# Optimization experiments

Measured on AMD Instinct MI355X. Metric: run time of the kernel, lower is better.

Reference implementation:

```python
import jax, jax.numpy as jnp
import numpy as np

D_MODEL, D_HEAD, N_HEADS, N_KV_HEADS = 4096, 128, 32, 8
EPS = 1e-5
N = 2048


def rms_norm(x, w, eps):
    return x * jax.lax.rsqrt(jnp.mean(x * x, axis=-1, keepdims=True) + eps) * w


def rope_swap(x):
    # [x0, x1, x2, x3] -> [-x1, x0, -x3, x2]
    xp = x.reshape(x.shape[:-1] + (-1, 2))
    return jnp.stack([-xp[..., 1], xp[..., 0]], axis=-1).reshape(x.shape)


def rope_rotate(x, r_cos, r_sin):
    return x * r_cos + rope_swap(x) * r_sin


def setup_inputs() -> dict:
    key = jax.random.key(0)
    ks = jax.random.split(key, 8)
    sd = 1.0 / np.sqrt(D_MODEL)
    return {
        "x": jax.random.normal(ks[0], (N, D_MODEL), dtype=jnp.float32),
        "r_cos": jax.random.normal(ks[1], (N, D_HEAD), dtype=jnp.float32),
        "r_sin": jax.random.normal(ks[2], (N, D_HEAD), dtype=jnp.float32),
        "w_norm": jnp.ones((D_MODEL,), dtype=jnp.float32),
        "wq": jax.random.normal(ks[3], (D_MODEL, N_HEADS * D_HEAD), dtype=jnp.float32) * sd,
        "wk": jax.random.normal(ks[4], (D_MODEL, N_KV_HEADS * D_HEAD), dtype=jnp.float32) * sd,
        "wv": jax.random.normal(ks[5], (D_MODEL, N_KV_HEADS * D_HEAD), dtype=jnp.float32) * sd,
        "wo": jax.random.normal(ks[6], (D_MODEL, D_MODEL), dtype=jnp.float32) * sd,
    }


def reference(x, r_cos, r_sin, w_norm, wq, wk, wv, wo):
    n = x.shape[0]
    residual = x
    h = rms_norm(x, w_norm, EPS)

    # projections -> [n_heads, n, d_head]
    q = (h @ wq).reshape(n, N_HEADS, D_HEAD).transpose(1, 0, 2)
    k = (h @ wk).reshape(n, N_KV_HEADS, D_HEAD).transpose(1, 0, 2)
    v = (h @ wv).reshape(n, N_KV_HEADS, D_HEAD).transpose(1, 0, 2)

    # GQA: repeat kv heads
    reps = N_HEADS // N_KV_HEADS
    k = jnp.repeat(k, reps, axis=0)
    v = jnp.repeat(v, reps, axis=0)

    q = rope_rotate(q, r_cos, r_sin)
    k = rope_rotate(k, r_cos, r_sin)

    mask = jnp.where(
        jnp.tril(jnp.ones((n, n), dtype=bool)), 0.0, -jnp.inf
    ).astype(x.dtype)
    scores = jnp.einsum("hnd,hmd->hnm", q, k) / np.sqrt(D_HEAD).astype(np.float32) + mask
    a = jnp.einsum("hnm,hmd->hnd", jax.nn.softmax(scores, axis=-1), v)

    a = a.transpose(1, 0, 2).reshape(n, N_HEADS * D_HEAD)
    return residual + a @ wo
```

## Files before the change

kernel.cpp:

```cpp
#include <hip/hip_runtime.h>
#include <stdint.h>
#include <math.h>

#define TOK 2048
#define DMODEL 4096
#define QKV_LD 5120
#define KVB 64
#define PS_LD 72

typedef __attribute__((ext_vector_type(8))) short short8;
typedef __attribute__((ext_vector_type(4))) short short4v;
typedef __attribute__((ext_vector_type(8))) __bf16 bf16x8;
typedef __attribute__((ext_vector_type(4))) float f32x4;

__device__ __forceinline__ unsigned short f2bf(float f) {
  unsigned u = __float_as_uint(f);
  u += 0x7fffu + ((u >> 16) & 1u);
  return (unsigned short)(u >> 16);
}

__device__ __forceinline__ void gl16(const void* g, void* l) {
  __builtin_amdgcn_global_load_lds((__attribute__((address_space(1))) void*)g,
                                   (__attribute__((address_space(3))) void*)l,
                                   16, 0, 0);
}

__device__ __forceinline__ f32x4 mfma16(short8 a, short8 b, f32x4 c) {
  return __builtin_amdgcn_mfma_f32_16x16x32_bf16(__builtin_bit_cast(bf16x8, a),
                                                 __builtin_bit_cast(bf16x8, b),
                                                 c, 0, 0, 0);
}

__device__ __forceinline__ float fexp2(float x) {
  float r;
  asm("v_exp_f32 %0, %1" : "=v"(r) : "v"(x));
  return r;
}

template <int N>
__device__ __forceinline__ void waitvm() {
  if constexpr (N == 0) asm volatile("s_waitcnt vmcnt(0)" ::: "memory");
  else if constexpr (N == 3) asm volatile("s_waitcnt vmcnt(3)" ::: "memory");
  else if constexpr (N == 4) asm volatile("s_waitcnt vmcnt(4)" ::: "memory");
  else if constexpr (N == 8) asm volatile("s_waitcnt vmcnt(8)" ::: "memory");
  else static_assert(N == 0 || N == 3 || N == 4 || N == 8, "add literal");
}

__global__ __launch_bounds__(256) void k_rmsnorm(const float* __restrict__ x,
                                                 const float* __restrict__ w,
                                                 unsigned short* __restrict__ h) {
  const int row = blockIdx.x;
  const float* xr = x + (size_t)row * DMODEL;
  float4 v[4];
  float ss = 0.f;
#pragma unroll
  for (int i = 0; i < 4; ++i) {
    v[i] = *(const float4*)(xr + threadIdx.x * 4 + i * 1024);
    ss += v[i].x * v[i].x + v[i].y * v[i].y + v[i].z * v[i].z + v[i].w * v[i].w;
  }
#pragma unroll
  for (int m = 1; m < 64; m <<= 1) ss += __shfl_xor(ss, m, 64);
  __shared__ float ws4[4];
  if ((threadIdx.x & 63) == 0) ws4[threadIdx.x >> 6] = ss;
  __syncthreads();
  const float scale = rsqrtf((ws4[0] + ws4[1] + ws4[2] + ws4[3]) * (1.0f / DMODEL) + 1e-5f);
  unsigned short* hr = h + (size_t)row * DMODEL;
#pragma unroll
  for (int i = 0; i < 4; ++i) {
    int col = threadIdx.x * 4 + i * 1024;
    float4 wv = *(const float4*)(w + col);
    uint2 o;
    o.x = (unsigned)f2bf(v[i].x * scale * wv.x) | ((unsigned)f2bf(v[i].y * scale * wv.y) << 16);
    o.y = (unsigned)f2bf(v[i].z * scale * wv.z) | ((unsigned)f2bf(v[i].w * scale * wv.w) << 16);
    *(uint2*)(hr + col) = o;
  }
}

__global__ __launch_bounds__(256) void k_wconvert(const float* __restrict__ W,
                                                  unsigned short* __restrict__ WT,
                                                  int K, int N) {
  __shared__ unsigned short tile[64][65];
  const int n0 = blockIdx.x * 64, k0 = blockIdx.y * 64;
  const int t = threadIdx.x;
  {
    const int r = t >> 2, c0 = (t & 3) * 16;
    const float* src = W + (size_t)(k0 + r) * N + n0 + c0;
#pragma unroll
    for (int i = 0; i < 4; ++i) {
      float4 f = *(const float4*)(src + i * 4);
      tile[r][c0 + i * 4 + 0] = f2bf(f.x);
      tile[r][c0 + i * 4 + 1] = f2bf(f.y);
      tile[r][c0 + i * 4 + 2] = f2bf(f.z);
      tile[r][c0 + i * 4 + 3] = f2bf(f.w);
    }
  }
  __syncthreads();
  {
    const int n = t >> 2, c0 = (t & 3) * 16;
    unsigned short* dst = WT + (size_t)(n0 + n) * K + k0 + c0;
    unsigned short v[16];
#pragma unroll
    for (int i = 0; i < 16; ++i) v[i] = tile[c0 + i][n];
    uint4 o0, o1;
    o0.x = v[0] | ((unsigned)v[1] << 16);  o0.y = v[2] | ((unsigned)v[3] << 16);
    o0.z = v[4] | ((unsigned)v[5] << 16);  o0.w = v[6] | ((unsigned)v[7] << 16);
    o1.x = v[8] | ((unsigned)v[9] << 16);  o1.y = v[10] | ((unsigned)v[11] << 16);
    o1.z = v[12] | ((unsigned)v[13] << 16); o1.w = v[14] | ((unsigned)v[15] << 16);
    *(uint4*)dst = o0;
    *(uint4*)(dst + 8) = o1;
  }
}

__device__ __forceinline__ short8 rdfrag(const unsigned short* buf, int row, int kc) {
  return *(const short8*)((const char*)buf + row * 128 + ((kc ^ (row & 7)) << 4));
}

template <int BM, int BN, int HALF>
__device__ __forceinline__ void stage_half(const unsigned short* __restrict__ A,
                                           const unsigned short* __restrict__ BT,
                                           unsigned short* __restrict__ buf,
                                           int m0, int n0, int K, int kt, int tid) {
  constexpr int LA = BM / 64, LB = BN / 64;
  constexpr int H0A = LA / 2, H0B = (LB + 1) / 2;
  constexpr int A0 = HALF ? H0A : 0, A1 = HALF ? LA : H0A;
  constexpr int B0 = HALF ? H0B : 0, B1 = HALF ? LB : H0B;
  unsigned short* bbuf = buf + BM * 64;
#pragma unroll
  for (int i = A0; i < A1; ++i) {
    const int s = i * 512 + tid, row = s >> 3, ch = s & 7;
    gl16(A + (size_t)(m0 + row) * K + kt + ((ch ^ (row & 7)) << 3), (char*)buf + s * 16);
  }
#pragma unroll
  for (int i = B0; i < B1; ++i) {
    const int s = i * 512 + tid, row = s >> 3, ch = s & 7;
    gl16(BT + (size_t)(n0 + row) * K + kt + ((ch ^ (row & 7)) << 3), (char*)bbuf + s * 16);
  }
}

template <int BM, int BN, int MODE>
__global__ __launch_bounds__(512, 2) void k_gemm_big(const unsigned short* __restrict__ A,
                                                     const unsigned short* __restrict__ BT,
                                                     const float* __restrict__ resid,
                                                     void* __restrict__ Cout,
                                                     unsigned short* __restrict__ vtg,
                                                     const float* __restrict__ rc,
                                                     const float* __restrict__ rs,
                                                     int M, int N, int K) {
  extern __shared__ __align__(16) unsigned short lds[];
  constexpr int MREP = BM / 32;
  constexpr int NREP = BN / 64;
  constexpr int TILE = (BM + BN) * 64;
  constexpr int LA = BM / 64, LB = BN / 64;
  constexpr int H0 = LA / 2 + (LB + 1) / 2;

  const int tid = threadIdx.x, lane = tid & 63;
  const int w = tid >> 6, wm = w >> 2, wn = w & 3;
  const int lr = lane & 15, lh = lane >> 4;

  const int wg0 = blockIdx.x;
  const int xcd = wg0 & 7, l = wg0 >> 3;
  const int m0 = (((xcd >> 2) << 2) + (l >> 3)) * BM;
  const int n0 = (((xcd & 3) << 3) + (l & 7)) * BN;

  const f32x4 zf = {0.f, 0.f, 0.f, 0.f};
  f32x4 acc[MREP][NREP];
#pragma unroll
  for (int i = 0; i < MREP; ++i) {
#pragma unroll
    for (int j = 0; j < NREP; ++j) acc[i][j] = zf;
  }

  const int arow0 = wm * (BM / 2);
  const int brow0 = wn * (BN / 4);
  const int NT = K >> 6;
  int cur = 0;

  stage_half<BM, BN, 0>(A, BT, lds, m0, n0, K, 0, tid);
  stage_half<BM, BN, 1>(A, BT, lds, m0, n0, K, 0, tid);

  for (int t = 0; t < NT; ++t) {
    const unsigned short* abuf = lds + cur * TILE;
    const unsigned short* bbuf = abuf + BM * 64;
    unsigned short* nbuf = lds + (cur ^ 1) * TILE;
    const bool pre = (t + 1 < NT);
    const int ktn = (t + 1) << 6;

    short8 bfr[NREP], afr[4];
    if (pre) {
      stage_half<BM, BN, 0>(A, BT, nbuf, m0, n0, K, ktn, tid);
      waitvm<H0>();
    } else {
      waitvm<0>();
    }
    __builtin_amdgcn_s_barrier();
#pragma unroll
    for (int nr = 0; nr < NREP; ++nr) bfr[nr] = rdfrag(bbuf, brow0 + nr * 16 + lr, lh);
#pragma unroll
    for (int mi = 0; mi < 4; ++mi) afr[mi] = rdfrag(abuf, arow0 + mi * 16 + lr, lh);
    __builtin_amdgcn_s_setprio(1);
#pragma unroll
    for (int mi = 0; mi < 4; ++mi) {
#pragma unroll
      for (int nr = 0; nr < NREP; ++nr)
        acc[mi][nr] = mfma16(afr[mi], bfr[nr], acc[mi][nr]);
    }
    __builtin_amdgcn_s_setprio(0);
    if (pre) stage_half<BM, BN, 1>(A, BT, nbuf, m0, n0, K, ktn, tid);
#pragma unroll
    for (int mi = 0; mi < 4; ++mi) afr[mi] = rdfrag(abuf, arow0 + (4 + mi) * 16 + lr, lh);
    __builtin_amdgcn_s_setprio(1);
#pragma unroll
    for (int mi = 0; mi < 4; ++mi) {
#pragma unroll
      for (int nr = 0; nr < NREP; ++nr)
        acc[4 + mi][nr] = mfma16(afr[mi], bfr[nr], acc[4 + mi][nr]);
    }
    __builtin_amdgcn_s_setprio(0);
#pragma unroll
    for (int nr = 0; nr < NREP; ++nr) bfr[nr] = rdfrag(bbuf, brow0 + nr * 16 + lr, 4 + lh);
#pragma unroll
    for (int mi = 0; mi < 4; ++mi) afr[mi] = rdfrag(abuf, arow0 + mi * 16 + lr, 4 + lh);
    __builtin_amdgcn_s_setprio(1);
#pragma unroll
    for (int mi = 0; mi < 4; ++mi) {
#pragma unroll
      for (int nr = 0; nr < NREP; ++nr)
        acc[mi][nr] = mfma16(afr[mi], bfr[nr], acc[mi][nr]);
    }
    __builtin_amdgcn_s_setprio(0);
#pragma unroll
    for (int mi = 0; mi < 4; ++mi) afr[mi] = rdfrag(abuf, arow0 + (4 + mi) * 16 + lr, 4 + lh);
    asm volatile("s_waitcnt lgkmcnt(0)" ::: "memory");
    __builtin_amdgcn_s_barrier();
    __builtin_amdgcn_s_setprio(1);
#pragma unroll
    for (int mi = 0; mi < 4; ++mi) {
#pragma unroll
      for (int nr = 0; nr < NREP; ++nr)
        acc[4 + mi][nr] = mfma16(afr[mi], bfr[nr], acc[4 + mi][nr]);
    }
    __builtin_amdgcn_s_setprio(0);
    cur ^= 1;
  }

#pragma unroll
  for (int ai = 0; ai < MREP; ++ai) {
#pragma unroll
    for (int ni = 0; ni < NREP; ++ni) {
      const int colg = n0 + wn * (BN / 4) + ni * 16 + lr;
      const int rowg0 = m0 + wm * (BM / 2) + ai * 16 + 4 * lh;
      if (MODE == 1) {
#pragma unroll
        for (int r = 0; r < 4; ++r)
          ((float*)Cout)[(size_t)(rowg0 + r) * N + colg] =
              acc[ai][ni][r] + resid[(size_t)(rowg0 + r) * N + colg];
      } else if (colg >= 5120) {
        short4v o;
#pragma unroll
        for (int r = 0; r < 4; ++r) o[r] = (short)f2bf(acc[ai][ni][r]);
        *(short4v*)(vtg + (size_t)(colg - 5120) * TOK + rowg0) = o;
      } else {
        const int d = colg & 127;
#pragma unroll
        for (int r = 0; r < 4; ++r) {
          const int row = rowg0 + r;
          const float v = acc[ai][ni][r];
          const float p = __shfl_xor(v, 1, 64);
          const float c = rc[row * 128 + d];
          const float s = rs[row * 128 + d];
          const float y = (lr & 1) ? fmaf(p, s, v * c) : fmaf(-p, s, v * c);
          ((unsigned short*)Cout)[(size_t)row * QKV_LD + colg] = f2bf(y);
        }
      }
    }
  }
}

__global__ __launch_bounds__(256) void k_attn(const unsigned short* __restrict__ qkv,
                                              const unsigned short* __restrict__ vtg,
                                              unsigned short* __restrict__ aout) {
  extern __shared__ __align__(16) unsigned short sm[];
  unsigned short* const KsB = sm;
  unsigned short* const VtB = sm + 2 * KVB * 128;
  unsigned short* const Ps = sm + 4 * KVB * 128;
  const int head = blockIdx.y;
  const int hkv = head >> 2;
  const int tid = threadIdx.x, lane = tid & 63, w = tid >> 6;
  const int lr = lane & 15, lh = lane >> 4;
  const float scale2 = 0.08838834764831845f * 1.44269504088896340736f;
  const f32x4 zf = {0.f, 0.f, 0.f, 0.f};

  for (int half = 0; half < 2; ++half) {
    const int qt = half ? (31 - blockIdx.x) : blockIdx.x;
    const int q0 = qt * 64;

    short8 qf[4];
    {
      const unsigned short* qbase = qkv + (size_t)(q0 + w * 16 + lr) * QKV_LD + head * 128;
#pragma unroll
      for (int kd = 0; kd < 4; ++kd) qf[kd] = *(const short8*)(qbase + kd * 32 + lh * 8);
    }
    f32x4 oacc[8];
#pragma unroll
    for (int vt = 0; vt < 8; ++vt) oacc[vt] = zf;
    float Mr[4], Lr[4];
#pragma unroll
    for (int r = 0; r < 4; ++r) { Mr[r] = -INFINITY; Lr[r] = 0.f; }

    const int nt = qt + 1;
    int cur = 0;

    {
#pragma unroll
      for (int c = 0; c < 4; ++c) {
        const int s = c * 256 + w * 64 + lane;
        const int row = s >> 4, cp = s & 15;
        gl16(qkv + (size_t)row * QKV_LD + 4096 + hkv * 128 + ((cp ^ (row & 7)) * 8),
             (char*)KsB + (c * 256 + w * 64) * 16);
      }
#pragma unroll
      for (int c = 0; c < 4; ++c) {
        const int s = c * 256 + w * 64 + lane;
        const int row = s >> 3, cp = s & 7;
        gl16(vtg + (size_t)(hkv * 128 + row) * TOK + ((cp ^ (row & 7)) * 8),
             (char*)VtB + (c * 256 + w * 64) * 16);
      }
    }

    for (int t = 0; t < nt; ++t) {
      const unsigned short* Ks = KsB + cur * (KVB * 128);
      const unsigned short* Vt = VtB + cur * (128 * KVB);
      const int kv0 = t * KVB;
      if (t + 1 < nt) {
        unsigned short* Ksn = KsB + (cur ^ 1) * (KVB * 128);
        unsigned short* Vtn = VtB + (cur ^ 1) * (128 * KVB);
        const int kvn = (t + 1) * KVB;
#pragma unroll
        for (int c = 0; c < 4; ++c) {
          const int s = c * 256 + w * 64 + lane;
          const int row = s >> 4, cp = s & 15;
          gl16(qkv + (size_t)(kvn + row) * QKV_LD + 4096 + hkv * 128 + ((cp ^ (row & 7)) * 8),
               (char*)Ksn + (c * 256 + w * 64) * 16);
        }
#pragma unroll
        for (int c = 0; c < 4; ++c) {
          const int s = c * 256 + w * 64 + lane;
          const int row = s >> 3, cp = s & 7;
          gl16(vtg + (size_t)(hkv * 128 + row) * TOK + kvn + ((cp ^ (row & 7)) * 8),
               (char*)Vtn + (c * 256 + w * 64) * 16);
        }
        waitvm<8>();
      } else {
        waitvm<0>();
      }
      __builtin_amdgcn_s_barrier();

      f32x4 sacc[4];
#pragma unroll
      for (int ct = 0; ct < 4; ++ct) {
        sacc[ct] = zf;
        const int row = ct * 16 + lr;
#pragma unroll
        for (int kd = 0; kd < 4; ++kd) {
          const short8 kf = *(const short8*)((const char*)Ks + row * 256 +
                                             (((kd * 4 + lh) ^ (row & 7)) * 16));
          sacc[ct] = mfma16(qf[kd], kf, sacc[ct]);
        }
      }

      float scv[4], pv[4][4];
#pragma unroll
      for (int r = 0; r < 4; ++r) {
        const int qrow = q0 + w * 16 + 4 * lh + r;
        float s0 = sacc[0][r] * scale2;
        float s1 = sacc[1][r] * scale2;
        float s2 = sacc[2][r] * scale2;
        float s3 = sacc[3][r] * scale2;
        if (kv0 + lr > qrow) s0 = -INFINITY;
        if (kv0 + 16 + lr > qrow) s1 = -INFINITY;
        if (kv0 + 32 + lr > qrow) s2 = -INFINITY;
        if (kv0 + 48 + lr > qrow) s3 = -INFINITY;
        float tmax = fmaxf(fmaxf(s0, s1), fmaxf(s2, s3));
        tmax = fmaxf(tmax, __shfl_xor(tmax, 1, 16));
        tmax = fmaxf(tmax, __shfl_xor(tmax, 2, 16));
        tmax = fmaxf(tmax, __shfl_xor(tmax, 4, 16));
        tmax = fmaxf(tmax, __shfl_xor(tmax, 8, 16));
        const float mnew = fmaxf(Mr[r], tmax);
        const float sc = fexp2(Mr[r] - mnew);
        Mr[r] = mnew;
        const float p0 = fexp2(s0 - mnew);
        const float p1 = fexp2(s1 - mnew);
        const float p2 = fexp2(s2 - mnew);
        const float p3 = fexp2(s3 - mnew);
        float ps = (p0 + p1) + (p2 + p3);
        ps += __shfl_xor(ps, 1, 16);
        ps += __shfl_xor(ps, 2, 16);
        ps += __shfl_xor(ps, 4, 16);
        ps += __shfl_xor(ps, 8, 16);
        Lr[r] = Lr[r] * sc + ps;
        scv[r] = sc;
        pv[r][0] = p0; pv[r][1] = p1; pv[r][2] = p2; pv[r][3] = p3;
      }
#pragma unroll
      for (int vt = 0; vt < 8; ++vt) {
#pragma unroll
        for (int r = 0; r < 4; ++r) oacc[vt][r] *= scv[r];
      }

      unsigned short* pw = Ps + w * (16 * PS_LD);
#pragma unroll
      for (int r = 0; r < 4; ++r) {
#pragma unroll
        for (int ct = 0; ct < 4; ++ct)
          pw[(4 * lh + r) * PS_LD + ct * 16 + lr] = f2bf(pv[r][ct]);
      }
      asm volatile("s_waitcnt lgkmcnt(0)" ::: "memory");
      short8 pf[2];
      pf[0] = *(const short8*)(pw + lr * PS_LD + lh * 8);
      pf[1] = *(const short8*)(pw + lr * PS_LD + 32 + lh * 8);
      __builtin_amdgcn_s_setprio(1);
#pragma unroll
      for (int vt = 0; vt < 8; ++vt) {
        const int d = vt * 16 + lr;
#pragma unroll
        for (int kb = 0; kb < 2; ++kb) {
          const short8 vf = *(const short8*)((const char*)Vt + d * 128 +
                                             (((kb * 4 + lh) ^ (lr & 7)) * 16));
          oacc[vt] = mfma16(pf[kb], vf, oacc[vt]);
        }
      }
      __builtin_amdgcn_s_setprio(0);
      asm volatile("s_waitcnt lgkmcnt(0)" ::: "memory");
      __builtin_amdgcn_s_barrier();
      cur ^= 1;
    }

#pragma unroll
    for (int r = 0; r < 4; ++r) {
      const float inv = 1.0f / Lr[r];
      const size_t rowoff = (size_t)(q0 + w * 16 + 4 * lh + r) * DMODEL + head * 128;
#pragma unroll
      for (int vt = 0; vt < 8; ++vt)
        aout[rowoff + vt * 16 + lr] = f2bf(oacc[vt][r] * inv);
    }
  }
}

extern "C" void kernel_launch(void* const* d_in, const int* in_sizes, int n_in,
                              void* d_out, int out_size, void* d_ws, size_t ws_size,
                              hipStream_t stream) {
  (void)in_sizes; (void)n_in; (void)out_size; (void)ws_size;
  const float* x     = (const float*)d_in[0];
  const float* r_cos = (const float*)d_in[1];
  const float* r_sin = (const float*)d_in[2];
  const float* wnorm = (const float*)d_in[3];
  const float* wq    = (const float*)d_in[4];
  const float* wk    = (const float*)d_in[5];
  const float* wv    = (const float*)d_in[6];
  const float* wo    = (const float*)d_in[7];

  unsigned short* bufA = (unsigned short*)d_ws;
  unsigned short* qkvb = bufA + (size_t)TOK * DMODEL;
  unsigned short* wT   = qkvb + (size_t)TOK * QKV_LD;
  unsigned short* vtg  = wT + (size_t)6144 * DMODEL;

  hipFuncSetAttribute((const void*)k_gemm_big<256, 192, 0>,
                      hipFuncAttributeMaxDynamicSharedMemorySize, 4 * (256 + 192) * 64);
  hipFuncSetAttribute((const void*)k_gemm_big<256, 128, 1>,
                      hipFuncAttributeMaxDynamicSharedMemorySize, 4 * (256 + 128) * 64);
  const int attn_lds = 4 * KVB * 128 * 2 + 4 * 16 * PS_LD * 2;
  hipFuncSetAttribute((const void*)k_attn,
                      hipFuncAttributeMaxDynamicSharedMemorySize, attn_lds);

  k_rmsnorm<<<TOK, 256, 0, stream>>>(x, wnorm, bufA);
  k_wconvert<<<dim3(64, 64), 256, 0, stream>>>(wq, wT, DMODEL, 4096);
  k_wconvert<<<dim3(16, 64), 256, 0, stream>>>(wk, wT + (size_t)4096 * DMODEL, DMODEL, 1024);
  k_wconvert<<<dim3(16, 64), 256, 0, stream>>>(wv, wT + (size_t)5120 * DMODEL, DMODEL, 1024);
  k_gemm_big<256, 192, 0><<<dim3(256), 512, 4 * (256 + 192) * 64, stream>>>(
      bufA, wT, nullptr, qkvb, vtg, r_cos, r_sin, TOK, 6144, DMODEL);
  k_wconvert<<<dim3(64, 64), 256, 0, stream>>>(wo, wT, DMODEL, 4096);
  k_attn<<<dim3(16, 32), 256, attn_lds, stream>>>(qkvb, vtg, bufA);
  k_gemm_big<256, 128, 1><<<dim3(256), 512, 4 * (256 + 128) * 64, stream>>>(
      bufA, wT, x, d_out, nullptr, nullptr, nullptr, TOK, DMODEL, DMODEL);
}
```

Before: 325.8 us.

## Defer softmax rescaling with threshold, skip masking off-diagonal, defer row-sum reduction

Reworks the online softmax in the attention inner loop. The causal mask is now applied only on the diagonal tile. The running max is updated, and the output accumulator rescaled, only when some row's new max exceeds the stored max by more than 8 (log2 domain), checked wave-uniformly with __all. The per-row sum is kept as per-lane partials and reduced across lanes once at the end rather than every tile. This removes the shuffle reductions and the 32 multiplies per tile, at the cost of letting exp2 values grow up to 2^8 before rescaling, which bounds precision in bf16 P.

After: 309.6 us. 5.0% less time.

```diff
diff --git a/kernel.cpp b/kernel.cpp
--- a/kernel.cpp
+++ b/kernel.cpp
@@ -303,9 +303,9 @@
     f32x4 oacc[8];
 #pragma unroll
     for (int vt = 0; vt < 8; ++vt) oacc[vt] = zf;
-    float Mr[4], Lr[4];
-#pragma unroll
-    for (int r = 0; r < 4; ++r) { Mr[r] = -INFINITY; Lr[r] = 0.f; }
+    float Mr[4], Lp[4];
+#pragma unroll
+    for (int r = 0; r < 4; ++r) { Mr[r] = -INFINITY; Lp[r] = 0.f; }
 
     const int nt = qt + 1;
     int cur = 0;
@@ -368,43 +368,55 @@
         }
       }
 
-      float scv[4], pv[4][4];
+      const bool diag = (t == qt);
+      float sv[4][4], gmax[4];
 #pragma unroll
       for (int r = 0; r < 4; ++r) {
-        const int qrow = q0 + w * 16 + 4 * lh + r;
         float s0 = sacc[0][r] * scale2;
         float s1 = sacc[1][r] * scale2;
         float s2 = sacc[2][r] * scale2;
         float s3 = sacc[3][r] * scale2;
-        if (kv0 + lr > qrow) s0 = -INFINITY;
-        if (kv0 + 16 + lr > qrow) s1 = -INFINITY;
-        if (kv0 + 32 + lr > qrow) s2 = -INFINITY;
-        if (kv0 + 48 + lr > qrow) s3 = -INFINITY;
+        if (diag) {
+          const int qrow = q0 + w * 16 + 4 * lh + r;
+          if (kv0 + lr > qrow) s0 = -INFINITY;
+          if (kv0 + 16 + lr > qrow) s1 = -INFINITY;
+          if (kv0 + 32 + lr > qrow) s2 = -INFINITY;
+          if (kv0 + 48 + lr > qrow) s3 = -INFINITY;
+        }
         float tmax = fmaxf(fmaxf(s0, s1), fmaxf(s2, s3));
         tmax = fmaxf(tmax, __shfl_xor(tmax, 1, 16));
         tmax = fmaxf(tmax, __shfl_xor(tmax, 2, 16));
         tmax = fmaxf(tmax, __shfl_xor(tmax, 4, 16));
         tmax = fmaxf(tmax, __shfl_xor(tmax, 8, 16));
-        const float mnew = fmaxf(Mr[r], tmax);
-        const float sc = fexp2(Mr[r] - mnew);
-        Mr[r] = mnew;
-        const float p0 = fexp2(s0 - mnew);
-        const float p1 = fexp2(s1 - mnew);
-        const float p2 = fexp2(s2 - mnew);
-        const float p3 = fexp2(s3 - mnew);
-        float ps = (p0 + p1) + (p2 + p3);
-        ps += __shfl_xor(ps, 1, 16);
-        ps += __shfl_xor(ps, 2, 16);
-        ps += __shfl_xor(ps, 4, 16);
-        ps += __shfl_xor(ps, 8, 16);
-        Lr[r] = Lr[r] * sc + ps;
-        scv[r] = sc;
+        gmax[r] = tmax;
+        sv[r][0] = s0; sv[r][1] = s1; sv[r][2] = s2; sv[r][3] = s3;
+      }
+      const int cond = (gmax[0] <= Mr[0] + 8.f) && (gmax[1] <= Mr[1] + 8.f) &&
+                       (gmax[2] <= Mr[2] + 8.f) && (gmax[3] <= Mr[3] + 8.f);
+      if (!__all(cond)) {
+        float scv[4];
+#pragma unroll
+        for (int r = 0; r < 4; ++r) {
+          const float mnew = fmaxf(Mr[r], gmax[r]);
+          scv[r] = fexp2(Mr[r] - mnew);
+          Mr[r] = mnew;
+          Lp[r] *= scv[r];
+        }
+#pragma unroll
+        for (int vt = 0; vt < 8; ++vt) {
+#pragma unroll
+          for (int r = 0; r < 4; ++r) oacc[vt][r] *= scv[r];
+        }
+      }
+      float pv[4][4];
+#pragma unroll
+      for (int r = 0; r < 4; ++r) {
+        const float p0 = fexp2(sv[r][0] - Mr[r]);
+        const float p1 = fexp2(sv[r][1] - Mr[r]);
+        const float p2 = fexp2(sv[r][2] - Mr[r]);
+        const float p3 = fexp2(sv[r][3] - Mr[r]);
+        Lp[r] += (p0 + p1) + (p2 + p3);
         pv[r][0] = p0; pv[r][1] = p1; pv[r][2] = p2; pv[r][3] = p3;
-      }
-#pragma unroll
-      for (int vt = 0; vt < 8; ++vt) {
-#pragma unroll
-        for (int r = 0; r < 4; ++r) oacc[vt][r] *= scv[r];
       }
 
       unsigned short* pw = Ps + w * (16 * PS_LD);
@@ -437,7 +449,12 @@
 
 #pragma unroll
     for (int r = 0; r < 4; ++r) {
-      const float inv = 1.0f / Lr[r];
+      float Ls = Lp[r];
+      Ls += __shfl_xor(Ls, 1, 16);
+      Ls += __shfl_xor(Ls, 2, 16);
+      Ls += __shfl_xor(Ls, 4, 16);
+      Ls += __shfl_xor(Ls, 8, 16);
+      const float inv = 1.0f / Ls;
       const size_t rowoff = (size_t)(q0 + w * 16 + 4 * lh + r) * DMODEL + head * 128;
 #pragma unroll
       for (int vt = 0; vt < 8; ++vt)
```
